# Performance work log

Hardware: AMD Instinct MI355X
Metric: run time of the kernel (lower is better)

## Reference

```python
import jax, jax.numpy as jnp
import numpy as np

B, S, D, H = 2, 2048, 1024, 8
DH = D // H          # hidden_dim == attn_dim == 128
TOTAL = 4 * D        # (2*hidden_dim + 2*attn_dim) * H
EPS = 1e-5
ROPE_BASE = 10000.0


def _layernorm(x, g, b):
    m = jnp.mean(x, axis=-1, keepdims=True)
    v = jnp.mean(jnp.square(x - m), axis=-1, keepdims=True)
    return (x - m) * jax.lax.rsqrt(v + EPS) * g + b


def _rope(x):
    # x: [B, H, S, DH], interleaved even/odd RoPE as in the torch module
    half = DH // 2
    inv_freq = 1.0 / (ROPE_BASE ** (jnp.arange(0, DH, 2, dtype=jnp.float32) / DH))  # [half]
    t = jnp.arange(x.shape[2], dtype=jnp.float32)
    freqs = t[:, None] * inv_freq[None, :]                 # [S, half]
    cos = jnp.cos(freqs)[None, None, :, :]                 # [1,1,S,half]
    sin = jnp.sin(freqs)[None, None, :, :]
    xe, xo = x[..., 0::2], x[..., 1::2]
    re = xe * cos - xo * sin
    ro = xe * sin + xo * cos
    return jnp.stack([re, ro], axis=-1).reshape(x.shape)


def setup_inputs() -> dict:
    key = jax.random.key(0)
    ks = jax.random.split(key, 6)
    x = jax.random.normal(ks[0], (B, S, D), dtype=jnp.float32)
    attention_mask = jnp.ones((B, S), dtype=bool)
    # weights stored [in, out] so forward is x @ W + b
    w_uvqk = 0.02 * jax.random.normal(ks[1], (D, TOTAL), dtype=jnp.float32)
    b_uvqk = jnp.zeros((TOTAL,), dtype=jnp.float32)
    w_out = 0.02 * jax.random.normal(ks[2], (3 * D, D), dtype=jnp.float32)
    b_out = jnp.zeros((D,), dtype=jnp.float32)
    ln1_g = jnp.ones((D,), dtype=jnp.float32)
    ln1_b = jnp.zeros((D,), dtype=jnp.float32)
    ln2_g = jnp.ones((D,), dtype=jnp.float32)
    ln2_b = jnp.zeros((D,), dtype=jnp.float32)
    return {"x": x, "attention_mask": attention_mask,
            "ln1_g": ln1_g, "ln1_b": ln1_b,
            "w_uvqk": w_uvqk, "b_uvqk": b_uvqk,
            "ln2_g": ln2_g, "ln2_b": ln2_b,
            "w_out": w_out, "b_out": b_out}


def reference(x, attention_mask, ln1_g, ln1_b, w_uvqk, b_uvqk, ln2_g, ln2_b, w_out, b_out):
    normed = _layernorm(x, ln1_g, ln1_b)
    uvqk = jax.nn.silu(normed @ w_uvqk + b_uvqk)          # [B,S,4D]
    u, v, q, k = jnp.split(uvqk, [D, 2 * D, 3 * D], axis=-1)
    q = q.reshape(B, S, H, DH).transpose(0, 2, 1, 3)      # [B,H,S,DH]
    k = k.reshape(B, S, H, DH).transpose(0, 2, 1, 3)
    v = v.reshape(B, S, H, DH).transpose(0, 2, 1, 3)
    q, k = _rope(q), _rope(k)
    scale = jnp.float32(DH) ** 0.5
    scores = jnp.einsum('bhsd,bhtd->bhst', q, k) / scale  # [B,H,S,S] fp32
    causal = jnp.tril(jnp.ones((S, S), dtype=bool))
    pad = attention_mask[:, None, :, None] & attention_mask[:, None, None, :]
    valid = pad & causal[None, None, :, :]
    scores = jnp.where(valid, scores, jnp.float32(-30.0))
    scores = jnp.clip(scores, -30.0, 30.0)
    attn = jax.nn.silu(scores)                            # SiLU instead of softmax
    ao = jnp.einsum('bhst,bhtd->bhsd', attn, v)           # [B,H,S,DH]
    ao = ao.transpose(0, 2, 1, 3).reshape(B, S, D)
    normed_attn = _layernorm(ao, ln2_g, ln2_b)
    cat = jnp.concatenate([u, ao, normed_attn * u], axis=-1)  # [B,S,3D]
    return x + (cat @ w_out + b_out)
```

## Files before the change

### kernel.cpp

```cpp
#include <hip/hip_runtime.h>
#include <hip/hip_bf16.h>
#include <math.h>

#define Bm 2
#define Sm 2048
#define Dm 1024
#define Hm 8
#define DHm 128
#define TOTALm 4096
#define ROWS (Bm*Sm)
#define K2m (3*Dm)

typedef __bf16 bf16;
typedef __bf16 bf16x8 __attribute__((ext_vector_type(8)));
typedef __bf16 bf16x4 __attribute__((ext_vector_type(4)));
typedef float  f32x4  __attribute__((ext_vector_type(4)));

__device__ __forceinline__ void stage_tile_128x32(
    const bf16* __restrict__ g, int ld, bf16* lds, int tid)
{
    int wid = tid >> 6;
    #pragma unroll
    for (int j = 0; j < 2; j++) {
        int e0  = (j*256 + tid) * 8;
        int row = e0 >> 5, col = e0 & 31;
        const bf16* src = g + (size_t)row*ld + col;
        bf16* dst = lds + (size_t)(j*256 + wid*64)*8;
        __builtin_amdgcn_global_load_lds(
            (const __attribute__((address_space(1))) unsigned int*)src,
            (__attribute__((address_space(3))) unsigned int*)dst,
            16, 0, 0);
    }
}

__device__ __forceinline__ void stage_tile_64x32(
    const bf16* __restrict__ g, int ld, bf16* lds, int tid)
{
    int wid = tid >> 6;
    int e0 = tid * 8;
    int row = e0 >> 5, col = e0 & 31;
    const bf16* src = g + (size_t)row*ld + col;
    bf16* dst = lds + (size_t)wid*512;
    __builtin_amdgcn_global_load_lds(
        (const __attribute__((address_space(1))) unsigned int*)src,
        (__attribute__((address_space(3))) unsigned int*)dst,
        16, 0, 0);
}

__global__ __launch_bounds__(256) void prep_kernel(
    const float* __restrict__ x, const float* __restrict__ g1,
    const float* __restrict__ b1, bf16* __restrict__ normed,
    const float* __restrict__ w_uvqk, bf16* __restrict__ Wt1,
    const float* __restrict__ w_out,  bf16* __restrict__ Wt2,
    float* __restrict__ ct, float* __restrict__ st)
{
    __shared__ float tile[32][33];
    __shared__ float red[4];
    __shared__ float stats[2];
    int bid = blockIdx.x;
    int tid = threadIdx.x;
    if (bid < 7168) {
        const float* in; bf16* out; int R, C, bx, by;
        if (bid < 4096) { in = w_uvqk; out = Wt1; R = Dm;  C = TOTALm; bx = bid & 127; by = bid >> 7; }
        else { int id2 = bid - 4096; in = w_out; out = Wt2; R = K2m; C = Dm; bx = id2 & 31; by = id2 >> 5; }
        int c0 = bx*32, r0 = by*32;
        int tx = tid & 31, ty = tid >> 5;
        for (int i=0;i<4;i++) {
            int r = ty + i*8;
            tile[r][tx] = in[(size_t)(r0+r)*C + c0+tx];
        }
        __syncthreads();
        for (int i=0;i<4;i++) {
            int cl = ty + i*8;
            out[(size_t)(c0+cl)*R + r0+tx] = (bf16)tile[tx][cl];
        }
    } else if (bid < 7680) {
        int idx = (bid - 7168)*256 + tid;
        int t = idx >> 6, p = idx & 63;
        float inv = expf(-0.143911568f * (float)p);
        float f = (float)t * inv;
        float sv, cv;
        sincosf(f, &sv, &cv);
        ct[idx] = cv; st[idx] = sv;
    } else {
        int row = bid - 7680;
        const float* xr = x + (size_t)row * Dm;
        float4 v = *(const float4*)(xr + tid*4);
        float s = v.x+v.y+v.z+v.w;
        for (int o=32;o>0;o>>=1) s += __shfl_down(s,o);
        int wid = tid>>6, lane = tid&63;
        if (lane==0) red[wid]=s;
        __syncthreads();
        if (tid==0) stats[0] = (red[0]+red[1]+red[2]+red[3]) * (1.f/Dm);
        __syncthreads();
        float m = stats[0];
        float d0=v.x-m,d1=v.y-m,d2=v.z-m,d3=v.w-m;
        float q = d0*d0+d1*d1+d2*d2+d3*d3;
        for (int o=32;o>0;o>>=1) q += __shfl_down(q,o);
        if (lane==0) red[wid]=q;
        __syncthreads();
        if (tid==0) stats[1] = rsqrtf((red[0]+red[1]+red[2]+red[3])*(1.f/Dm) + 1e-5f);
        __syncthreads();
        float rs = stats[1];
        float4 gv = *(const float4*)(g1 + tid*4);
        float4 bv = *(const float4*)(b1 + tid*4);
        bf16x4 o;
        o[0] = (bf16)(d0*rs*gv.x + bv.x);
        o[1] = (bf16)(d1*rs*gv.y + bv.y);
        o[2] = (bf16)(d2*rs*gv.z + bv.z);
        o[3] = (bf16)(d3*rs*gv.w + bv.w);
        *(bf16x4*)(normed + (size_t)row*Dm + tid*4) = o;
    }
}

__global__ __launch_bounds__(256,4) void gemm1_kernel(
    const bf16* __restrict__ A, const bf16* __restrict__ Bt,
    const float* __restrict__ bias,
    const float* __restrict__ ct, const float* __restrict__ st,
    bf16* __restrict__ cat, bf16* __restrict__ qb, bf16* __restrict__ kb,
    bf16* __restrict__ vt)
{
    __shared__ __align__(16) bf16 sm[17408];
    const int K = Dm;
    int m0 = blockIdx.y*128, n0 = blockIdx.x*128;
    int tid = threadIdx.x, wid = tid>>6, lane = tid&63;
    int quad = lane>>4, l16 = lane&15;
    int wm = (wid>>1)*64, wn = (wid&1)*64;
    f32x4 acc[4][4] = {};
    bf16* sA = sm;
    bf16* sB = sm + 8192;
    for (int k0=0;k0<K;k0+=64) {
        __syncthreads();
        stage_tile_128x32(A  + (size_t)m0*K + k0,      K, sA,        tid);
        stage_tile_128x32(A  + (size_t)m0*K + k0 + 32, K, sA + 4096, tid);
        stage_tile_128x32(Bt + (size_t)n0*K + k0,      K, sB,        tid);
        stage_tile_128x32(Bt + (size_t)n0*K + k0 + 32, K, sB + 4096, tid);
        __syncthreads();
        #pragma unroll
        for (int kc=0;kc<2;kc++) {
            bf16x8 af[4], bfr[4];
            #pragma unroll
            for (int t=0;t<4;t++) af[t]  = *(const bf16x8*)&sA[kc*4096 + (wm+t*16+l16)*32 + quad*8];
            #pragma unroll
            for (int t=0;t<4;t++) bfr[t] = *(const bf16x8*)&sB[kc*4096 + (wn+t*16+l16)*32 + quad*8];
            #pragma unroll
            for (int tm=0;tm<4;tm++)
                #pragma unroll
                for (int tn=0;tn<4;tn++)
                    acc[tm][tn] = __builtin_amdgcn_mfma_f32_16x16x32_bf16(af[tm], bfr[tn], acc[tm][tn], 0,0,0);
        }
    }
    int sect = n0 >> 10;
    if (sect == 1) {
        __syncthreads();
        #pragma unroll
        for (int tm=0;tm<4;tm++)
        #pragma unroll
        for (int tn=0;tn<4;tn++) {
            int colg = n0 + wn + tn*16 + l16;
            float bval = bias[colg];
            int d = colg & 127;
            #pragma unroll
            for (int r=0;r<4;r++) {
                int srow = wm + tm*16 + quad*4 + r;
                float val = acc[tm][tn][r] + bval;
                val = val / (1.f + __expf(-val));
                sm[d*136 + srow] = (bf16)val;
            }
        }
        __syncthreads();
        int h = (n0 >> 7) & 7;
        int b = m0 >> 11, s0l = m0 & 2047;
        int d2 = tid >> 1, sh = (tid & 1)*64;
        bf16* dst = vt + ((size_t)(b*Hm+h)*DHm + d2)*Sm + s0l + sh;
        const bf16* srcl = &sm[d2*136 + sh];
        #pragma unroll
        for (int i=0;i<8;i++)
            *(bf16x8*)(dst + i*8) = *(const bf16x8*)(srcl + i*8);
    } else if (sect == 0) {
        #pragma unroll
        for (int tm=0;tm<4;tm++)
        #pragma unroll
        for (int tn=0;tn<4;tn++) {
            int c = n0 + wn + tn*16 + l16;
            float bval = bias[c];
            #pragma unroll
            for (int r=0;r<4;r++) {
                int row = m0 + wm + tm*16 + quad*4 + r;
                float val = acc[tm][tn][r] + bval;
                val = val / (1.f + __expf(-val));
                cat[(size_t)row*K2m + c] = (bf16)val;
            }
        }
    } else {
        bf16* dstb = (sect==2) ? qb : kb;
        float postscale = (sect==2) ? 0.08838834764831845f : 1.0f;
        #pragma unroll
        for (int tm=0;tm<4;tm++)
        #pragma unroll
        for (int tn=0;tn<4;tn++) {
            int colg = n0 + wn + tn*16 + l16;
            int c = colg & 1023;
            int h = c>>7, d = c&127, p = d>>1;
            float bval = bias[colg];
            #pragma unroll
            for (int r=0;r<4;r++) {
                int row = m0 + wm + tm*16 + quad*4 + r;
                float val = acc[tm][tn][r] + bval;
                val = val / (1.f + __expf(-val));
                int b = row>>11, s = row&2047;
                float pv = __shfl_xor(val, 1);
                float cv = ct[s*64+p], sv = st[s*64+p];
                float res = (d&1) ? (pv*sv + val*cv) : (val*cv - pv*sv);
                dstb[((size_t)(b*Hm+h)*Sm + s)*DHm + d] = (bf16)(res * postscale);
            }
        }
    }
}

__global__ __launch_bounds__(256,3) void attn_kernel(
    const bf16* __restrict__ qb, const bf16* __restrict__ kb,
    const bf16* __restrict__ vt, float* __restrict__ ao0,
    float* __restrict__ ao1)
{
    __shared__ __align__(16) bf16 sK[16384];
    __shared__ __align__(16) bf16 P[64*136];
    int bid = blockIdx.x;
    int head = bid & 15;
    int idx = bid >> 4;
    int b = head >> 3, h = head & 7;
    int qt, k_begin, k_end;
    float* aoOut;
    if (idx < 32) {
        qt = 31 - (idx >> 1);
        int nkt = (qt >> 1) + 1;
        int half = (nkt + 1) >> 1;
        if ((idx & 1) == 0) { k_begin = 0;    k_end = half; aoOut = ao0; }
        else                { k_begin = half; k_end = nkt;  aoOut = ao1; }
    } else {
        qt = idx - 32;
        k_begin = 0; k_end = (qt >> 1) + 1;
        aoOut = ao0;
    }
    const size_t headoff = (size_t)(b*Hm+h)*Sm*DHm;
    const bf16* Q  = qb + headoff;
    const bf16* Km = kb + headoff;
    const bf16* V  = vt + headoff;
    int tid=threadIdx.x, wid=tid>>6, lane=tid&63, quad=lane>>4, l16=lane&15;
    int wm=(wid>>1)*32, wn=(wid&1)*64;
    int q0 = qt*64;
    f32x4 accO[2][4] = {};
    bf16x8 qf[4][2];
    #pragma unroll
    for (int kc=0;kc<4;kc++)
        #pragma unroll
        for (int t=0;t<2;t++)
            qf[kc][t] = *(const bf16x8*)(Q + (size_t)(q0+wm+t*16+l16)*DHm + kc*32 + quad*8);
    {
        int t0 = k_begin*128;
        #pragma unroll
        for (int kc=0;kc<4;kc++)
            stage_tile_128x32(Km + (size_t)t0*DHm + kc*32, DHm, sK + kc*4096, tid);
    }
    for (int kt=k_begin; kt<k_end; kt++) {
        int t0 = kt*128;
        asm volatile("s_waitcnt vmcnt(0)" ::: "memory");
        __builtin_amdgcn_s_barrier();
        bool clean = (t0 + 127 <= q0);
        #pragma unroll
        for (int ts=0; ts<4; ts++) {
            f32x4 accS[2] = {};
            __builtin_amdgcn_s_setprio(1);
            #pragma unroll
            for (int kc=0;kc<4;kc++) {
                bf16x8 bfr = *(const bf16x8*)&sK[kc*4096 + (wn+ts*16+l16)*32 + quad*8];
                #pragma unroll
                for (int tm=0;tm<2;tm++)
                    accS[tm] = __builtin_amdgcn_mfma_f32_16x16x32_bf16(qf[kc][tm], bfr, accS[tm], 0,0,0);
            }
            __builtin_amdgcn_s_setprio(0);
            #pragma unroll
            for (int tm=0;tm<2;tm++)
                #pragma unroll
                for (int r=0;r<4;r++) {
                    int srow = wm+tm*16+quad*4+r;
                    int tcol = wn+ts*16+l16;
                    float s = fminf(30.f, accS[tm][r]);
                    float p = s * __builtin_amdgcn_rcpf(1.f + __expf(-s));
                    if (!clean && (t0+tcol > q0+srow)) p = 0.f;
                    P[srow*136 + tcol] = (bf16)p;
                }
        }
        asm volatile("s_waitcnt lgkmcnt(0)" ::: "memory");
        __builtin_amdgcn_s_barrier();
        if (kt+1 < k_end) {
            int t0n = t0 + 128;
            #pragma unroll
            for (int kc=0;kc<4;kc++)
                stage_tile_128x32(Km + (size_t)t0n*DHm + kc*32, DHm, sK + kc*4096, tid);
        }
        int kcn = ((q0 + 63 - t0) >> 5) + 1;
        if (kcn > 4) kcn = 4;
        #pragma unroll
        for (int kc=0;kc<4;kc++) {
            if (kc < kcn) {
                bf16x8 af[2], bfr[4];
                #pragma unroll
                for (int t=0;t<2;t++) af[t]  = *(const bf16x8*)&P[(wm+t*16+l16)*136 + kc*32 + quad*8];
                #pragma unroll
                for (int t=0;t<4;t++) bfr[t] = *(const bf16x8*)(V + (size_t)(wn+t*16+l16)*Sm + t0 + kc*32 + quad*8);
                __builtin_amdgcn_s_setprio(1);
                #pragma unroll
                for (int tm=0;tm<2;tm++)
                    #pragma unroll
                    for (int tn=0;tn<4;tn++)
                        accO[tm][tn] = __builtin_amdgcn_mfma_f32_16x16x32_bf16(af[tm], bfr[tn], accO[tm][tn], 0,0,0);
                __builtin_amdgcn_s_setprio(0);
            }
        }
    }
    #pragma unroll
    for (int tm=0;tm<2;tm++)
    #pragma unroll
    for (int tn=0;tn<4;tn++)
        #pragma unroll
        for (int r=0;r<4;r++) {
            int s = q0+wm+tm*16+quad*4+r;
            int d = wn+tn*16+l16;
            aoOut[((size_t)(b*Sm+s))*Dm + h*DHm + d] = accO[tm][tn][r];
        }
}

__global__ __launch_bounds__(256) void ln2_cat_kernel(
    const float* __restrict__ ao0, const float* __restrict__ ao1,
    const float* __restrict__ g,
    const float* __restrict__ bb, bf16* __restrict__ cat)
{
    int row = blockIdx.x;
    int tid = threadIdx.x;
    int s = row & 2047;
    float4 v  = *(const float4*)(ao0 + (size_t)row*Dm + tid*4);
    if (s >= 1024) {
        float4 v1 = *(const float4*)(ao1 + (size_t)row*Dm + tid*4);
        v.x += v1.x; v.y += v1.y; v.z += v1.z; v.w += v1.w;
    }
    float ssum = v.x+v.y+v.z+v.w;
    for (int o=32;o>0;o>>=1) ssum += __shfl_down(ssum,o);
    __shared__ float red[4]; __shared__ float stats[2];
    int wid = tid>>6, lane = tid&63;
    if (lane==0) red[wid]=ssum;
    __syncthreads();
    if (tid==0) stats[0] = (red[0]+red[1]+red[2]+red[3]) * (1.f/Dm);
    __syncthreads();
    float m = stats[0];
    float d0=v.x-m,d1=v.y-m,d2=v.z-m,d3=v.w-m;
    float q = d0*d0+d1*d1+d2*d2+d3*d3;
    for (int o=32;o>0;o>>=1) q += __shfl_down(q,o);
    if (lane==0) red[wid]=q;
    __syncthreads();
    if (tid==0) stats[1] = rsqrtf((red[0]+red[1]+red[2]+red[3])*(1.f/Dm) + 1e-5f);
    __syncthreads();
    float rs = stats[1];
    float4 gv = *(const float4*)(g + tid*4);
    float4 bv = *(const float4*)(bb + tid*4);
    bf16* crow = cat + (size_t)row * K2m;
    bf16x4 u4 = *(const bf16x4*)(crow + tid*4);
    bf16x4 a4, nu4;
    a4[0]=(bf16)v.x; a4[1]=(bf16)v.y; a4[2]=(bf16)v.z; a4[3]=(bf16)v.w;
    nu4[0]=(bf16)(((v.x-m)*rs*gv.x+bv.x) * (float)u4[0]);
    nu4[1]=(bf16)(((v.y-m)*rs*gv.y+bv.y) * (float)u4[1]);
    nu4[2]=(bf16)(((v.z-m)*rs*gv.z+bv.z) * (float)u4[2]);
    nu4[3]=(bf16)(((v.w-m)*rs*gv.w+bv.w) * (float)u4[3]);
    *(bf16x4*)(crow + 1024 + tid*4) = a4;
    *(bf16x4*)(crow + 2048 + tid*4) = nu4;
}

__global__ __launch_bounds__(256,4) void gemm2_kernel(
    const bf16* __restrict__ A, const bf16* __restrict__ Bt,
    const float* __restrict__ bias, const float* __restrict__ x,
    float* __restrict__ out)
{
    __shared__ __align__(16) bf16 sm[12288];
    const int K = K2m, N = Dm;
    int m0 = blockIdx.y*128, n0 = blockIdx.x*64;
    int tid = threadIdx.x, wid = tid>>6, lane = tid&63;
    int quad = lane>>4, l16 = lane&15;
    int wm = (wid>>1)*64, wn = (wid&1)*32;
    f32x4 acc[4][2] = {};
    bf16* sA = sm;
    bf16* sB = sm + 8192;
    for (int k0=0;k0<K;k0+=64) {
        __syncthreads();
        stage_tile_128x32(A  + (size_t)m0*K + k0,      K, sA,        tid);
        stage_tile_128x32(A  + (size_t)m0*K + k0 + 32, K, sA + 4096, tid);
        stage_tile_64x32 (Bt + (size_t)n0*K + k0,      K, sB,        tid);
        stage_tile_64x32 (Bt + (size_t)n0*K + k0 + 32, K, sB + 2048, tid);
        __syncthreads();
        #pragma unroll
        for (int kc=0;kc<2;kc++) {
            bf16x8 af[4], bfr[2];
            #pragma unroll
            for (int t=0;t<4;t++) af[t]  = *(const bf16x8*)&sm[kc*4096 + (wm+t*16+l16)*32 + quad*8];
            #pragma unroll
            for (int t=0;t<2;t++) bfr[t] = *(const bf16x8*)&sB[kc*2048 + (wn+t*16+l16)*32 + quad*8];
            #pragma unroll
            for (int tm=0;tm<4;tm++)
                #pragma unroll
                for (int tn=0;tn<2;tn++)
                    acc[tm][tn] = __builtin_amdgcn_mfma_f32_16x16x32_bf16(af[tm], bfr[tn], acc[tm][tn], 0,0,0);
        }
    }
    #pragma unroll
    for (int tm=0;tm<4;tm++)
    #pragma unroll
    for (int tn=0;tn<2;tn++) {
        int col = n0 + wn + tn*16 + l16;
        float bval = bias[col];
        #pragma unroll
        for (int r=0;r<4;r++) {
            int row = m0 + wm + tm*16 + quad*4 + r;
            out[(size_t)row*N + col] = acc[tm][tn][r] + bval + x[(size_t)row*N + col];
        }
    }
}

extern "C" void kernel_launch(void* const* d_in, const int* in_sizes, int n_in,
                              void* d_out, int out_size, void* d_ws, size_t ws_size,
                              hipStream_t stream)
{
    const float* x      = (const float*)d_in[0];
    const float* ln1_g  = (const float*)d_in[2];
    const float* ln1_b  = (const float*)d_in[3];
    const float* w_uvqk = (const float*)d_in[4];
    const float* b_uvqk = (const float*)d_in[5];
    const float* ln2_g  = (const float*)d_in[6];
    const float* ln2_b  = (const float*)d_in[7];
    const float* w_out  = (const float*)d_in[8];
    const float* b_out  = (const float*)d_in[9];

    char* w = (char*)d_ws;
    bf16*  normed = (bf16*)(w);
    bf16*  Wt1    = (bf16*)(w + 8388608);
    bf16*  Wt2    = (bf16*)(w + 16777216);
    bf16*  qb     = (bf16*)(w + 23068672);
    bf16*  kb     = (bf16*)(w + 31457280);
    bf16*  vt     = (bf16*)(w + 39845888);
    float* ao0    = (float*)(w + 48234496);
    bf16*  cat    = (bf16*)(w + 65011712);
    float* ct     = (float*)(w + 90177536);
    float* st     = (float*)(w + 90701824);
    float* ao1    = (float*)(w);

    prep_kernel<<<11776, 256, 0, stream>>>(x, ln1_g, ln1_b, normed,
                                           w_uvqk, Wt1, w_out, Wt2, ct, st);
    gemm1_kernel<<<dim3(TOTALm/128, ROWS/128), 256, 0, stream>>>(
        normed, Wt1, b_uvqk, ct, st, cat, qb, kb, vt);
    attn_kernel<<<768, 256, 0, stream>>>(qb, kb, vt, ao0, ao1);
    ln2_cat_kernel<<<ROWS, 256, 0, stream>>>(ao0, ao1, ln2_g, ln2_b, cat);
    gemm2_kernel<<<dim3(Dm/64, ROWS/128), 256, 0, stream>>>(
        cat, Wt2, b_out, x, (float*)d_out);
}
```

Measured before the change: 264.8 us.

## Split long causal attention rows into three key segments with atomic merge

Reworks the attention work split so the longest query tiles (qt 20-31) run as three key-range segments, middle tiles (10-19) as two, and short ones as one, going from 768 to 1056 blocks. Segments beyond the first atomically add into a zeroed ao1 buffer, which needs two new memsets, and ln2 now sums ao1 from row 640 on. It also register-prefetches the V fragments for the next k-chunk ahead of the barrier to hide global load latency. This balances load across CUs at the cost of atomics, memset launches and more partial-sum traffic.

```diff
diff --git a/kernel.cpp b/kernel.cpp
--- a/kernel.cpp
+++ b/kernel.cpp
@@ -227,21 +227,25 @@
     __shared__ __align__(16) bf16 P[64*136];
     int bid = blockIdx.x;
     int head = bid & 15;
-    int idx = bid >> 4;
+    int u = bid >> 4;
     int b = head >> 3, h = head & 7;
-    int qt, k_begin, k_end;
-    float* aoOut;
-    if (idx < 32) {
-        qt = 31 - (idx >> 1);
-        int nkt = (qt >> 1) + 1;
-        int half = (nkt + 1) >> 1;
-        if ((idx & 1) == 0) { k_begin = 0;    k_end = half; aoOut = ao0; }
-        else                { k_begin = half; k_end = nkt;  aoOut = ao1; }
-    } else {
-        qt = idx - 32;
-        k_begin = 0; k_end = (qt >> 1) + 1;
-        aoOut = ao0;
-    }
+    int qt, seg, nseg;
+    if (u < 36)      { qt = 31 - (u/3);          seg = u - (31-qt)*3; nseg = 3; }
+    else if (u < 56) { int w2 = u - 36; qt = 19 - (w2>>1); seg = w2 & 1; nseg = 2; }
+    else             { qt = 9 - (u - 56);        seg = 0;             nseg = 1; }
+    int nkt = (qt>>1) + 1;
+    int k_begin, k_end;
+    if (nseg == 1)      { k_begin = 0; k_end = nkt; }
+    else if (nseg == 2) { int s0 = (nkt+1)>>1;
+                          if (seg==0) { k_begin = 0;  k_end = s0; }
+                          else        { k_begin = s0; k_end = nkt; } }
+    else { int base = nkt/3, rem = nkt - base*3;
+           int l0 = base + (rem>0 ? 1:0), l1 = base + (rem>1 ? 1:0);
+           if (seg==0)      { k_begin = 0;     k_end = l0; }
+           else if (seg==1) { k_begin = l0;    k_end = l0+l1; }
+           else             { k_begin = l0+l1; k_end = nkt; } }
+    bool atomic_out = (nseg==3) && (seg>0);
+    float* aoOut = (seg==0) ? ao0 : ao1;
     const size_t headoff = (size_t)(b*Hm+h)*Sm*DHm;
     const bf16* Q  = qb + headoff;
     const bf16* Km = kb + headoff;
@@ -291,6 +295,12 @@
                     P[srow*136 + tcol] = (bf16)p;
                 }
         }
+        int kcn = ((q0 + 63 - t0) >> 5) + 1;
+        if (kcn > 4) kcn = 4;
+        bf16x8 vnext[4];
+        #pragma unroll
+        for (int t=0;t<4;t++)
+            vnext[t] = *(const bf16x8*)(V + (size_t)(wn+t*16+l16)*Sm + t0 + quad*8);
         asm volatile("s_waitcnt lgkmcnt(0)" ::: "memory");
         __builtin_amdgcn_s_barrier();
         if (kt+1 < k_end) {
@@ -299,16 +309,20 @@
             for (int kc=0;kc<4;kc++)
                 stage_tile_128x32(Km + (size_t)t0n*DHm + kc*32, DHm, sK + kc*4096, tid);
         }
-        int kcn = ((q0 + 63 - t0) >> 5) + 1;
-        if (kcn > 4) kcn = 4;
         #pragma unroll
         for (int kc=0;kc<4;kc++) {
             if (kc < kcn) {
-                bf16x8 af[2], bfr[4];
-                #pragma unroll
-                for (int t=0;t<2;t++) af[t]  = *(const bf16x8*)&P[(wm+t*16+l16)*136 + kc*32 + quad*8];
-                #pragma unroll
-                for (int t=0;t<4;t++) bfr[t] = *(const bf16x8*)(V + (size_t)(wn+t*16+l16)*Sm + t0 + kc*32 + quad*8);
+                bf16x8 bfr[4];
+                #pragma unroll
+                for (int t=0;t<4;t++) bfr[t] = vnext[t];
+                if (kc+1 < kcn) {
+                    #pragma unroll
+                    for (int t=0;t<4;t++)
+                        vnext[t] = *(const bf16x8*)(V + (size_t)(wn+t*16+l16)*Sm + t0 + (kc+1)*32 + quad*8);
+                }
+                bf16x8 af[2];
+                #pragma unroll
+                for (int t=0;t<2;t++) af[t] = *(const bf16x8*)&P[(wm+t*16+l16)*136 + kc*32 + quad*8];
                 __builtin_amdgcn_s_setprio(1);
                 #pragma unroll
                 for (int tm=0;tm<2;tm++)
@@ -327,7 +341,9 @@
         for (int r=0;r<4;r++) {
             int s = q0+wm+tm*16+quad*4+r;
             int d = wn+tn*16+l16;
-            aoOut[((size_t)(b*Sm+s))*Dm + h*DHm + d] = accO[tm][tn][r];
+            size_t off = ((size_t)(b*Sm+s))*Dm + h*DHm + d;
+            if (atomic_out) unsafeAtomicAdd(&aoOut[off], accO[tm][tn][r]);
+            else            aoOut[off] = accO[tm][tn][r];
         }
 }
 
@@ -340,7 +356,7 @@
     int tid = threadIdx.x;
     int s = row & 2047;
     float4 v  = *(const float4*)(ao0 + (size_t)row*Dm + tid*4);
-    if (s >= 1024) {
+    if (s >= 640) {
         float4 v1 = *(const float4*)(ao1 + (size_t)row*Dm + tid*4);
         v.x += v1.x; v.y += v1.y; v.z += v1.z; v.w += v1.w;
     }
@@ -400,7 +416,7 @@
         for (int kc=0;kc<2;kc++) {
             bf16x8 af[4], bfr[2];
             #pragma unroll
-            for (int t=0;t<4;t++) af[t]  = *(const bf16x8*)&sm[kc*4096 + (wm+t*16+l16)*32 + quad*8];
+            for (int t=0;t<4;t++) af[t]  = *(const bf16x8*)&sA[kc*4096 + (wm+t*16+l16)*32 + quad*8];
             #pragma unroll
             for (int t=0;t<2;t++) bfr[t] = *(const bf16x8*)&sB[kc*2048 + (wn+t*16+l16)*32 + quad*8];
             #pragma unroll
@@ -455,7 +471,9 @@
                                            w_uvqk, Wt1, w_out, Wt2, ct, st);
     gemm1_kernel<<<dim3(TOTALm/128, ROWS/128), 256, 0, stream>>>(
         normed, Wt1, b_uvqk, ct, st, cat, qb, kb, vt);
-    attn_kernel<<<768, 256, 0, stream>>>(qb, kb, vt, ao0, ao1);
+    hipMemsetAsync(w + (size_t)1310720*4, 0, (size_t)786432*4, stream);
+    hipMemsetAsync(w + (size_t)3407872*4, 0, (size_t)786432*4, stream);
+    attn_kernel<<<1056, 256, 0, stream>>>(qb, kb, vt, ao0, ao1);
     ln2_cat_kernel<<<ROWS, 256, 0, stream>>>(ao0, ao1, ln2_g, ln2_b, cat);
     gemm2_kernel<<<dim3(Dm/64, ROWS/128), 256, 0, stream>>>(
         cat, Wt2, b_out, x, (float*)d_out);
```

New measurement: 270.6 us. 2.2% more time.

## Use 8 waves per attention block, XOR-swizzle K tile in LDS, prefetch V

Applied to the files above, without the earlier changes.

The attention kernel now runs 512 threads (8 waves) per block, each wave owning a 32x32 output slice instead of 32x64, so fewer accumulators live per thread and more waves can hide latency. K tiles are staged into LDS with an XOR column swizzle to reduce bank conflicts on the B-fragment reads. V fragments are software-prefetched one k-chunk ahead from global memory. The trade-off is more barrier participants and duplicated Q fragment loads per block, with occupancy set by launch_bounds(512,6). A gemm2 sm-vs-sA read is renamed, which is equivalent.

```diff
diff --git a/kernel.cpp b/kernel.cpp
--- a/kernel.cpp
+++ b/kernel.cpp
@@ -40,6 +40,21 @@
     int e0 = tid * 8;
     int row = e0 >> 5, col = e0 & 31;
     const bf16* src = g + (size_t)row*ld + col;
+    bf16* dst = lds + (size_t)wid*512;
+    __builtin_amdgcn_global_load_lds(
+        (const __attribute__((address_space(1))) unsigned int*)src,
+        (__attribute__((address_space(3))) unsigned int*)dst,
+        16, 0, 0);
+}
+
+__device__ __forceinline__ void stage_tile_128x32_sw512(
+    const bf16* __restrict__ g, int ld, bf16* lds, int tid)
+{
+    int wid = tid >> 6;
+    int row = tid >> 2;
+    int c   = tid & 3;
+    int csw = c ^ ((row >> 1) & 3);
+    const bf16* src = g + (size_t)row*ld + csw*8;
     bf16* dst = lds + (size_t)wid*512;
     __builtin_amdgcn_global_load_lds(
         (const __attribute__((address_space(1))) unsigned int*)src,
@@ -218,7 +233,7 @@
     }
 }
 
-__global__ __launch_bounds__(256,3) void attn_kernel(
+__global__ __launch_bounds__(512,6) void attn_kernel(
     const bf16* __restrict__ qb, const bf16* __restrict__ kb,
     const bf16* __restrict__ vt, float* __restrict__ ao0,
     float* __restrict__ ao1)
@@ -247,9 +262,9 @@
     const bf16* Km = kb + headoff;
     const bf16* V  = vt + headoff;
     int tid=threadIdx.x, wid=tid>>6, lane=tid&63, quad=lane>>4, l16=lane&15;
-    int wm=(wid>>1)*32, wn=(wid&1)*64;
+    int wm=(wid>>2)*32, wc=(wid&3)*32;
     int q0 = qt*64;
-    f32x4 accO[2][4] = {};
+    f32x4 accO[2][2] = {};
     bf16x8 qf[4][2];
     #pragma unroll
     for (int kc=0;kc<4;kc++)
@@ -260,7 +275,7 @@
         int t0 = k_begin*128;
         #pragma unroll
         for (int kc=0;kc<4;kc++)
-            stage_tile_128x32(Km + (size_t)t0*DHm + kc*32, DHm, sK + kc*4096, tid);
+            stage_tile_128x32_sw512(Km + (size_t)t0*DHm + kc*32, DHm, sK + kc*4096, tid);
     }
     for (int kt=k_begin; kt<k_end; kt++) {
         int t0 = kt*128;
@@ -268,12 +283,14 @@
         __builtin_amdgcn_s_barrier();
         bool clean = (t0 + 127 <= q0);
         #pragma unroll
-        for (int ts=0; ts<4; ts++) {
+        for (int ts=0; ts<2; ts++) {
             f32x4 accS[2] = {};
+            int rr = wc + ts*16 + l16;
+            int csw = (quad ^ ((rr>>1)&3))*8;
             __builtin_amdgcn_s_setprio(1);
             #pragma unroll
             for (int kc=0;kc<4;kc++) {
-                bf16x8 bfr = *(const bf16x8*)&sK[kc*4096 + (wn+ts*16+l16)*32 + quad*8];
+                bf16x8 bfr = *(const bf16x8*)&sK[kc*4096 + rr*32 + csw];
                 #pragma unroll
                 for (int tm=0;tm<2;tm++)
                     accS[tm] = __builtin_amdgcn_mfma_f32_16x16x32_bf16(qf[kc][tm], bfr, accS[tm], 0,0,0);
@@ -284,37 +301,47 @@
                 #pragma unroll
                 for (int r=0;r<4;r++) {
                     int srow = wm+tm*16+quad*4+r;
-                    int tcol = wn+ts*16+l16;
+                    int tcol = rr;
                     float s = fminf(30.f, accS[tm][r]);
                     float p = s * __builtin_amdgcn_rcpf(1.f + __expf(-s));
                     if (!clean && (t0+tcol > q0+srow)) p = 0.f;
                     P[srow*136 + tcol] = (bf16)p;
                 }
         }
+        int kcn = ((q0 + 63 - t0) >> 5) + 1;
+        if (kcn > 4) kcn = 4;
+        bf16x8 vnext[2];
+        #pragma unroll
+        for (int t=0;t<2;t++)
+            vnext[t] = *(const bf16x8*)(V + (size_t)(wc+t*16+l16)*Sm + t0 + quad*8);
         asm volatile("s_waitcnt lgkmcnt(0)" ::: "memory");
         __builtin_amdgcn_s_barrier();
         if (kt+1 < k_end) {
             int t0n = t0 + 128;
             #pragma unroll
             for (int kc=0;kc<4;kc++)
-                stage_tile_128x32(Km + (size_t)t0n*DHm + kc*32, DHm, sK + kc*4096, tid);
-        }
-        int kcn = ((q0 + 63 - t0) >> 5) + 1;
-        if (kcn > 4) kcn = 4;
+                stage_tile_128x32_sw512(Km + (size_t)t0n*DHm + kc*32, DHm, sK + kc*4096, tid);
+        }
         #pragma unroll
         for (int kc=0;kc<4;kc++) {
             if (kc < kcn) {
-                bf16x8 af[2], bfr[4];
-                #pragma unroll
-                for (int t=0;t<2;t++) af[t]  = *(const bf16x8*)&P[(wm+t*16+l16)*136 + kc*32 + quad*8];
-                #pragma unroll
-                for (int t=0;t<4;t++) bfr[t] = *(const bf16x8*)(V + (size_t)(wn+t*16+l16)*Sm + t0 + kc*32 + quad*8);
+                bf16x8 bfr2[2];
+                #pragma unroll
+                for (int t=0;t<2;t++) bfr2[t] = vnext[t];
+                if (kc+1 < kcn) {
+                    #pragma unroll
+                    for (int t=0;t<2;t++)
+                        vnext[t] = *(const bf16x8*)(V + (size_t)(wc+t*16+l16)*Sm + t0 + (kc+1)*32 + quad*8);
+                }
+                bf16x8 af[2];
+                #pragma unroll
+                for (int t=0;t<2;t++) af[t] = *(const bf16x8*)&P[(wm+t*16+l16)*136 + kc*32 + quad*8];
                 __builtin_amdgcn_s_setprio(1);
                 #pragma unroll
                 for (int tm=0;tm<2;tm++)
                     #pragma unroll
-                    for (int tn=0;tn<4;tn++)
-                        accO[tm][tn] = __builtin_amdgcn_mfma_f32_16x16x32_bf16(af[tm], bfr[tn], accO[tm][tn], 0,0,0);
+                    for (int tn=0;tn<2;tn++)
+                        accO[tm][tn] = __builtin_amdgcn_mfma_f32_16x16x32_bf16(af[tm], bfr2[tn], accO[tm][tn], 0,0,0);
                 __builtin_amdgcn_s_setprio(0);
             }
         }
@@ -322,11 +349,11 @@
     #pragma unroll
     for (int tm=0;tm<2;tm++)
     #pragma unroll
-    for (int tn=0;tn<4;tn++)
+    for (int tn=0;tn<2;tn++)
         #pragma unroll
         for (int r=0;r<4;r++) {
             int s = q0+wm+tm*16+quad*4+r;
-            int d = wn+tn*16+l16;
+            int d = wc+tn*16+l16;
             aoOut[((size_t)(b*Sm+s))*Dm + h*DHm + d] = accO[tm][tn][r];
         }
 }
@@ -400,7 +427,7 @@
         for (int kc=0;kc<2;kc++) {
             bf16x8 af[4], bfr[2];
             #pragma unroll
-            for (int t=0;t<4;t++) af[t]  = *(const bf16x8*)&sm[kc*4096 + (wm+t*16+l16)*32 + quad*8];
+            for (int t=0;t<4;t++) af[t]  = *(const bf16x8*)&sA[kc*4096 + (wm+t*16+l16)*32 + quad*8];
             #pragma unroll
             for (int t=0;t<2;t++) bfr[t] = *(const bf16x8*)&sB[kc*2048 + (wn+t*16+l16)*32 + quad*8];
             #pragma unroll
@@ -455,7 +482,7 @@
                                            w_uvqk, Wt1, w_out, Wt2, ct, st);
     gemm1_kernel<<<dim3(TOTALm/128, ROWS/128), 256, 0, stream>>>(
         normed, Wt1, b_uvqk, ct, st, cat, qb, kb, vt);
-    attn_kernel<<<768, 256, 0, stream>>>(qb, kb, vt, ao0, ao1);
+    attn_kernel<<<768, 512, 0, stream>>>(qb, kb, vt, ao0, ao1);
     ln2_cat_kernel<<<ROWS, 256, 0, stream>>>(ao0, ao1, ln2_g, ln2_b, cat);
     gemm2_kernel<<<dim3(Dm/64, ROWS/128), 256, 0, stream>>>(
         cat, Wt2, b_out, x, (float*)d_out);
```

Measured after the change: 283.6 us. 7.1% more time.
